# Kernel optimization log

Hardware: AMD Instinct MI355X
Metric: run time of the kernel (lower is better)

Reference implementation:

```python
import jax, jax.numpy as jnp
import numpy as np

B, T, I, H, O = 64, 1024, 512, 768, 512


def setup_inputs() -> dict:
    key = jax.random.key(0)
    ks = jax.random.split(key, 8)
    x_seq = jax.random.normal(ks[0], (B, T, I), dtype=jnp.float32)
    s = 0.02
    # Gate order along the 4H axis: f, i, g, o (matches the torch module's gates).
    Wx_f = jax.random.normal(ks[1], (4 * H, I), dtype=jnp.float32) * s
    Wh_f = jax.random.normal(ks[2], (4 * H, H), dtype=jnp.float32) * s
    Wx_b = jax.random.normal(ks[3], (4 * H, I), dtype=jnp.float32) * s
    Wh_b = jax.random.normal(ks[4], (4 * H, H), dtype=jnp.float32) * s
    # forget-gate bias init to 1.0 (f_Wxf.bias / b_Wxf.bias), rest 0
    b_gate = jnp.concatenate([jnp.ones((H,), jnp.float32), jnp.zeros((3 * H,), jnp.float32)])
    b_f = b_gate
    b_b = b_gate
    Why = jax.random.normal(ks[5], (O, 2 * H), dtype=jnp.float32) * s
    by = jnp.zeros((O,), jnp.float32)
    return {"x_seq": x_seq, "Wx_f": Wx_f, "Wh_f": Wh_f, "b_f": b_f,
            "Wx_b": Wx_b, "Wh_b": Wh_b, "b_b": b_b, "Why": Why, "by": by}


def _lstm_dir(x, Wx, Wh, b):
    # Precompute all input-to-gate projections in one fused GEMM over time.
    xp = jnp.einsum('bti,gi->btg', x, Wx) + b  # (B, T, 4H)

    def step(carry, xp_t):
        h, c = carry
        z = xp_t + h @ Wh.T                     # (B, 4H)
        f = jax.nn.sigmoid(z[:, 0 * H:1 * H])
        i = jax.nn.sigmoid(z[:, 1 * H:2 * H])
        g = jnp.tanh(z[:, 2 * H:3 * H])
        o = jax.nn.sigmoid(z[:, 3 * H:4 * H])
        c = f * c + i * g
        h = o * jnp.tanh(c)
        return (h, c), None

    h0 = jnp.zeros((x.shape[0], H), x.dtype)
    c0 = jnp.zeros((x.shape[0], H), x.dtype)
    (h, c), _ = jax.lax.scan(step, (h0, c0), jnp.swapaxes(xp, 0, 1))
    return h, c


def reference(x_seq, Wx_f, Wh_f, b_f, Wx_b, Wh_b, b_b, Why, by):
    h_fwd, c_fwd = _lstm_dir(x_seq, Wx_f, Wh_f, b_f)
    h_bwd, c_bwd = _lstm_dir(x_seq[:, ::-1, :], Wx_b, Wh_b, b_b)
    h_combined = jnp.concatenate([h_fwd, h_bwd], axis=1)  # (B, 2H)
    out = h_combined @ Why.T + by
    return out, h_fwd, c_fwd, h_bwd, c_bwd
```

## Files before the change

kernel.cpp:

```cpp
#include <hip/hip_runtime.h>
#include <hip/hip_cooperative_groups.h>

namespace cg = cooperative_groups;

#define B_ 64
#define T_ 1024
#define I_ 512
#define H_ 768
#define O_ 512
#define G4 3072
#define JB 16
#define NJ 48
#define NWGS 192

typedef short short8 __attribute__((ext_vector_type(8)));
typedef float f32x4 __attribute__((ext_vector_type(4)));
typedef int int4v __attribute__((ext_vector_type(4)));
typedef unsigned long long u64;

#define XBF_BYTES  (67108864)
#define WCAT_BYTES (15728640)
#define HBUF_BYTES (393216)

__device__ __forceinline__ unsigned short f32_to_bf16(float f) {
    union { float f; unsigned int u; } v; v.f = f;
    unsigned int r = v.u + 0x7fffu + ((v.u >> 16) & 1u);
    return (unsigned short)(r >> 16);
}
__device__ __forceinline__ float sigmoid_f(float x) { return 1.0f / (1.0f + __expf(-x)); }
__device__ __forceinline__ float tanh_f(float x) {
    float e = __expf(2.0f * x);
    return 1.0f - 2.0f / (e + 1.0f);
}

__device__ __forceinline__ void glds16(const void* g, void* l) {
    __builtin_amdgcn_global_load_lds(
        (const __attribute__((address_space(1))) unsigned int*)g,
        (__attribute__((address_space(3))) unsigned int*)l, 16, 0, 0);
}

__device__ __forceinline__ void ldsbar() {
    asm volatile("s_waitcnt lgkmcnt(0)" ::: "memory");
    __builtin_amdgcn_sched_barrier(0);
    __builtin_amdgcn_s_barrier();
    __builtin_amdgcn_sched_barrier(0);
}

__global__ void prep_x_kernel(const float* __restrict__ x, unsigned short* __restrict__ xb) {
    const size_t n = (size_t)B_ * T_ * 64;
    for (size_t i = (size_t)blockIdx.x * blockDim.x + threadIdx.x; i < n;
         i += (size_t)gridDim.x * blockDim.x) {
        int b  = (int)(i >> 16);
        int t  = (int)((i >> 6) & 1023);
        int kb = (int)(i & 63);
        const float4 v0 = *(const float4*)(x + i * 8);
        const float4 v1 = *(const float4*)(x + i * 8 + 4);
        short8 o;
        o[0] = (short)f32_to_bf16(v0.x); o[1] = (short)f32_to_bf16(v0.y);
        o[2] = (short)f32_to_bf16(v0.z); o[3] = (short)f32_to_bf16(v0.w);
        o[4] = (short)f32_to_bf16(v1.x); o[5] = (short)f32_to_bf16(v1.y);
        o[6] = (short)f32_to_bf16(v1.z); o[7] = (short)f32_to_bf16(v1.w);
        *(short8*)(xb + (((size_t)t * 64 + kb) * 64 + b) * 8) = o;
    }
}

__global__ void prep_w_kernel(const float* __restrict__ Wx_f, const float* __restrict__ Wh_f,
                              const float* __restrict__ Wx_b, const float* __restrict__ Wh_b,
                              unsigned short* __restrict__ w2, unsigned short* __restrict__ h2,
                              unsigned* __restrict__ bar) {
    const size_t n = (size_t)2 * G4 * 160;
    for (size_t i = (size_t)blockIdx.x * blockDim.x + threadIdx.x; i < n;
         i += (size_t)gridDim.x * blockDim.x) {
        int dir = (int)(i / 491520);
        int r2  = (int)(i % 491520);
        int row = r2 / 160;
        int kb  = r2 % 160;
        const float* Wx = dir ? Wx_b : Wx_f;
        const float* Wh = dir ? Wh_b : Wh_f;
        const float* src = (kb < 64) ? (Wx + (size_t)row * I_ + kb * 8)
                                     : (Wh + (size_t)row * H_ + (kb - 64) * 8);
        const float4 v0 = *(const float4*)(src);
        const float4 v1 = *(const float4*)(src + 4);
        short8 o;
        o[0] = (short)f32_to_bf16(v0.x); o[1] = (short)f32_to_bf16(v0.y);
        o[2] = (short)f32_to_bf16(v0.z); o[3] = (short)f32_to_bf16(v0.w);
        o[4] = (short)f32_to_bf16(v1.x); o[5] = (short)f32_to_bf16(v1.y);
        o[6] = (short)f32_to_bf16(v1.z); o[7] = (short)f32_to_bf16(v1.w);
        *(short8*)(w2 + (((size_t)dir * 160 + kb) * G4 + row) * 8) = o;
        if (i < 24576) {
            short8 z = {0,0,0,0,0,0,0,0};
            *(short8*)(h2 + i * 8) = z;
        }
        if (i < 512) bar[i] = 0u;
    }
}

__global__ void __launch_bounds__(512, 2)
bilstm_kernel(const float* __restrict__ bias_f, const float* __restrict__ bias_b,
              const unsigned short* __restrict__ xb, const unsigned short* __restrict__ w2,
              unsigned short* h2, unsigned* bar, float* d_out) {
    __shared__ unsigned short x_lds[64 * 32 * 8];
    __shared__ unsigned short h_lds[96 * 32 * 8];
    __shared__ float z_lds[4][32][17];
    __shared__ float c_tile[32][16];

    const int tid   = threadIdx.x;
    const int wg    = blockIdx.x;
    const int dir   = wg / 96;
    const int rem   = wg % 96;
    const int bh    = rem / NJ;
    const int jb    = rem % NJ;
    const int j0    = jb * JB;
    const int wave  = tid >> 6;
    const int lane  = tid & 63;
    const int gate  = wave & 3;
    const int mhalf = wave >> 2;
    const int quad  = lane >> 4;
    const int lrow  = lane & 15;
    const int m0l   = mhalf * 16 + lrow;

    c_tile[tid >> 4][tid & 15] = 0.0f;

    const float bias_r = (dir ? bias_b : bias_f)[gate * H_ + j0 + lrow];
    const int wrow = gate * H_ + j0 + lrow;

    const unsigned short* wx = w2 + (((size_t)dir * 160 + quad) * G4 + wrow) * 8;
    short8 wh[24];
#pragma unroll
    for (int ks = 0; ks < 24; ++ks)
        wh[ks] = *(const short8*)(w2 + (((size_t)dir * 160 + 64 + ks * 4 + quad) * G4 + wrow) * 8);

    const int group = dir * 2 + bh;
    unsigned* mybar = bar + (group * 4 + (jb & 3)) * 32;
    unsigned* barbase = bar + group * 4 * 32;

    const int src_off = (tid >> 5) * 1024 + bh * 512 + (tid & 31) * 16;

    char* const lds_wb   = (char*)x_lds + wave * 1024;
    char* const lds_mine = (char*)h_lds + tid * 16;
    const unsigned short* vax = x_lds + quad * 256 + m0l * 8;
    const unsigned short* vah = h_lds + quad * 256 + m0l * 8;

    {
        const int tx0 = dir ? (T_ - 1) : 0;
        const char* xsrc = (const char*)(xb + (size_t)tx0 * 32768) + src_off;
#pragma unroll
        for (int k = 0; k < 4; ++k) glds16(xsrc + k * 16384, lds_wb + k * 8192);
    }
    __syncthreads();

    for (int t = 0; t < T_; ++t) {
        const int pb = (t + 1) & 1;
        const int cb = t & 1;

        f32x4 acc0; acc0[0] = bias_r; acc0[1] = bias_r; acc0[2] = bias_r; acc0[3] = bias_r;

#pragma unroll
        for (int ks = 0; ks < 16; ++ks) {
            short8 a0 = *(const short8*)(vax + ks * 1024);
            short8 bf = *(const short8*)(wx + (size_t)ks * 4 * G4 * 8);
            acc0 = __builtin_amdgcn_mfma_f32_16x16x32_bf16(a0, bf, acc0, 0, 0, 0);
        }

        if (tid == 0) {
            const unsigned tgt = (unsigned)(NJ * t);
            for (;;) {
                unsigned ssum = 0;
#pragma unroll
                for (int i = 0; i < 4; ++i)
                    ssum += __hip_atomic_load(barbase + i * 32, __ATOMIC_RELAXED,
                                              __HIP_MEMORY_SCOPE_AGENT);
                if (ssum >= tgt) break;
                __builtin_amdgcn_s_sleep(1);
            }
        }
        asm volatile("" ::: "memory");
        __syncthreads();

        {
            const char* hp = (const char*)(h2 + (size_t)(dir * 2 + pb) * 49152) + src_off;
            int4v u0, u1, u2, u3, u4, u5;
#define HL(n) asm volatile("global_load_dwordx4 %0, %1, off sc1" : "=v"(u##n) : "v"(hp + (n) * 16384))
#define HS(n) *(int4v*)(lds_mine + (n) * 8192) = u##n
            HL(0); HL(1); HL(2); HL(3); HL(4); HL(5);
            asm volatile("s_waitcnt vmcnt(5)" ::: "memory"); HS(0);
            asm volatile("s_waitcnt vmcnt(4)" ::: "memory"); HS(1);
            asm volatile("s_waitcnt vmcnt(3)" ::: "memory"); HS(2);
            asm volatile("s_waitcnt vmcnt(2)" ::: "memory"); HS(3);
            asm volatile("s_waitcnt vmcnt(1)" ::: "memory"); HS(4);
            asm volatile("s_waitcnt vmcnt(0)" ::: "memory"); HS(5);
#undef HL
#undef HS
        }

        if (t + 1 < T_) {
            const int tx2 = dir ? (T_ - 2 - t) : (t + 1);
            const char* xsrc = (const char*)(xb + (size_t)tx2 * 32768) + src_off;
#pragma unroll
            for (int k = 0; k < 4; ++k) glds16(xsrc + k * 16384, lds_wb + k * 8192);
        }
        ldsbar();

#pragma unroll
        for (int ks = 0; ks < 24; ++ks) {
            short8 a0 = *(const short8*)(vah + ks * 1024);
            acc0 = __builtin_amdgcn_mfma_f32_16x16x32_bf16(a0, wh[ks], acc0, 0, 0, 0);
        }

#pragma unroll
        for (int r = 0; r < 4; ++r)
            z_lds[gate][mhalf * 16 + quad * 4 + r][lrow] = acc0[r];
        ldsbar();

        {
            unsigned short* hw = h2 + (size_t)(dir * 2 + cb) * 49152;
            const int gb  = tid >> 4;
            const int gj  = tid & 15;
            const int gjj = j0 + gj;
            const int bg  = bh * 32 + gb;
            float f0 = sigmoid_f(z_lds[0][gb][gj]);
            float i0 = sigmoid_f(z_lds[1][gb][gj]);
            float g0 = tanh_f(z_lds[2][gb][gj]);
            float o0 = sigmoid_f(z_lds[3][gb][gj]);
            float c0 = f0 * c_tile[gb][gj] + i0 * g0;
            c_tile[gb][gj] = c0;
            float h0 = o0 * tanh_f(c0);
            unsigned hv = (unsigned)f32_to_bf16(h0);
            unsigned ov = __shfl_xor(hv, 1);
            if (!(gj & 1)) {
                unsigned pack = hv | (ov << 16);
                unsigned* dst = (unsigned*)(hw + ((gjj >> 3) * 64 + bg) * 8 + (gjj & 7));
                __hip_atomic_store(dst, pack, __ATOMIC_RELAXED, __HIP_MEMORY_SCOPE_AGENT);
            }
            if (t == T_ - 1) {
                int hoff = 32768 + dir * 98304;
                d_out[hoff + bg * H_ + gjj]         = h0;
                d_out[hoff + 49152 + bg * H_ + gjj] = c0;
            }
        }
        __syncthreads();

        if (tid == 0)
            __hip_atomic_fetch_add(mybar, 1u, __ATOMIC_RELAXED, __HIP_MEMORY_SCOPE_AGENT);
    }
}

__global__ void proj_kernel(float* __restrict__ out, const float* __restrict__ Why,
                            const float* __restrict__ by) {
    __shared__ float hc[2 * H_];
    int b = blockIdx.x;
    const float* hf = out + 32768 + b * H_;
    const float* hb = out + 32768 + 98304 + b * H_;
    for (int i = threadIdx.x; i < H_; i += 256) { hc[i] = hf[i]; hc[H_ + i] = hb[i]; }
    __syncthreads();
    for (int o = threadIdx.x; o < O_; o += 256) {
        const float* wr = Why + (size_t)o * (2 * H_);
        float s = by[o];
        for (int k = 0; k < 2 * H_; k += 4) {
            float4 w = *(const float4*)(wr + k);
            s += w.x * hc[k] + w.y * hc[k + 1] + w.z * hc[k + 2] + w.w * hc[k + 3];
        }
        out[b * O_ + o] = s;
    }
}

extern "C" void kernel_launch(void* const* d_in, const int* in_sizes, int n_in,
                              void* d_out, int out_size, void* d_ws, size_t ws_size,
                              hipStream_t stream) {
    const float* x    = (const float*)d_in[0];
    const float* Wx_f = (const float*)d_in[1];
    const float* Wh_f = (const float*)d_in[2];
    const float* b_f  = (const float*)d_in[3];
    const float* Wx_b = (const float*)d_in[4];
    const float* Wh_b = (const float*)d_in[5];
    const float* b_b  = (const float*)d_in[6];
    const float* Why  = (const float*)d_in[7];
    const float* by   = (const float*)d_in[8];
    float* out = (float*)d_out;

    char* ws = (char*)d_ws;
    unsigned short* xbp = (unsigned short*)(ws);
    unsigned short* w2  = (unsigned short*)(ws + XBF_BYTES);
    unsigned short* h2  = (unsigned short*)(ws + XBF_BYTES + WCAT_BYTES);
    unsigned*       bar = (unsigned*)(ws + XBF_BYTES + WCAT_BYTES + HBUF_BYTES);

    prep_x_kernel<<<8192, 256, 0, stream>>>(x, xbp);
    prep_w_kernel<<<4096, 256, 0, stream>>>(Wx_f, Wh_f, Wx_b, Wh_b, w2, h2, bar);

    void* args[] = {(void*)&b_f, (void*)&b_b, (void*)&xbp, (void*)&w2,
                    (void*)&h2, (void*)&bar, (void*)&out};
    hipLaunchCooperativeKernel((void*)bilstm_kernel, dim3(NWGS), dim3(512), args, 0, stream);

    proj_kernel<<<B_, 256, 0, stream>>>(out, Why, by);
}
```

Baseline: 3.024 ms.

## Repartition BiLSTM workgroups into 16-batch by 32-unit tiles with split accumulators

Each workgroup now handles 16 batch rows and 32 hidden units across all four gates, instead of 32 batch rows and 16 units. That gives 8 independent groups (2 directions by 4 batch quarters), each synchronised by a 24-workgroup barrier instead of 48, and halves the recurrent h data each workgroup loads per step. The x-projection MFMAs are split around the barrier wait and the h global loads so they overlap the spin and load latency. Two accumulators alternate to break the MFMA dependency chain. In exchange, each workgroup now reads 128 weight rows spread across the four gate blocks.

```diff
diff --git a/kernel.cpp b/kernel.cpp
--- a/kernel.cpp
+++ b/kernel.cpp
@@ -9,14 +9,13 @@
 #define H_ 768
 #define O_ 512
 #define G4 3072
-#define JB 16
-#define NJ 48
+#define JB 32
+#define NJG 24
 #define NWGS 192
 
 typedef short short8 __attribute__((ext_vector_type(8)));
 typedef float f32x4 __attribute__((ext_vector_type(4)));
 typedef int int4v __attribute__((ext_vector_type(4)));
-typedef unsigned long long u64;
 
 #define XBF_BYTES  (67108864)
 #define WCAT_BYTES (15728640)
@@ -91,7 +90,7 @@
             short8 z = {0,0,0,0,0,0,0,0};
             *(short8*)(h2 + i * 8) = z;
         }
-        if (i < 512) bar[i] = 0u;
+        if (i < 1024) bar[i] = 0u;
     }
 }
 
@@ -99,30 +98,28 @@
 bilstm_kernel(const float* __restrict__ bias_f, const float* __restrict__ bias_b,
               const unsigned short* __restrict__ xb, const unsigned short* __restrict__ w2,
               unsigned short* h2, unsigned* bar, float* d_out) {
-    __shared__ unsigned short x_lds[64 * 32 * 8];
-    __shared__ unsigned short h_lds[96 * 32 * 8];
-    __shared__ float z_lds[4][32][17];
-    __shared__ float c_tile[32][16];
+    __shared__ unsigned short x_lds[64 * 16 * 8];
+    __shared__ unsigned short h_lds[96 * 16 * 8];
+    __shared__ float z_lds[16][132];
+    __shared__ float c_tile[16][32];
 
     const int tid   = threadIdx.x;
     const int wg    = blockIdx.x;
-    const int dir   = wg / 96;
-    const int rem   = wg % 96;
-    const int bh    = rem / NJ;
-    const int jb    = rem % NJ;
+    const int group = wg & 7;
+    const int jb    = wg >> 3;
+    const int dir   = group >> 2;
+    const int bq    = group & 3;
     const int j0    = jb * JB;
-    const int wave  = tid >> 6;
+    const int nt    = tid >> 6;
     const int lane  = tid & 63;
-    const int gate  = wave & 3;
-    const int mhalf = wave >> 2;
     const int quad  = lane >> 4;
     const int lrow  = lane & 15;
-    const int m0l   = mhalf * 16 + lrow;
-
-    c_tile[tid >> 4][tid & 15] = 0.0f;
-
-    const float bias_r = (dir ? bias_b : bias_f)[gate * H_ + j0 + lrow];
-    const int wrow = gate * H_ + j0 + lrow;
+    const int rl    = nt * 16 + lrow;
+
+    c_tile[tid >> 5][tid & 31] = 0.0f;
+
+    const int wrow = (rl >> 5) * H_ + j0 + (rl & 31);
+    const float bias_r = (dir ? bias_b : bias_f)[wrow];
 
     const unsigned short* wx = w2 + (((size_t)dir * 160 + quad) * G4 + wrow) * 8;
     short8 wh[24];
@@ -130,22 +127,21 @@
     for (int ks = 0; ks < 24; ++ks)
         wh[ks] = *(const short8*)(w2 + (((size_t)dir * 160 + 64 + ks * 4 + quad) * G4 + wrow) * 8);
 
-    const int group = dir * 2 + bh;
     unsigned* mybar = bar + (group * 4 + (jb & 3)) * 32;
-    unsigned* barbase = bar + group * 4 * 32;
-
-    const int src_off = (tid >> 5) * 1024 + bh * 512 + (tid & 31) * 16;
-
-    char* const lds_wb   = (char*)x_lds + wave * 1024;
-    char* const lds_mine = (char*)h_lds + tid * 16;
-    const unsigned short* vax = x_lds + quad * 256 + m0l * 8;
-    const unsigned short* vah = h_lds + quad * 256 + m0l * 8;
+    unsigned* barbase = bar + group * 128;
+
+    const int src_off = (tid >> 4) * 1024 + bq * 256 + (tid & 15) * 16;
+
+    char* const xdst = (char*)x_lds + nt * 1024;
+    char* const hdst = (char*)h_lds + tid * 16;
+    const unsigned short* vax = x_lds + quad * 128 + lrow * 8;
+    const unsigned short* vah = h_lds + quad * 128 + lrow * 8;
 
     {
         const int tx0 = dir ? (T_ - 1) : 0;
-        const char* xsrc = (const char*)(xb + (size_t)tx0 * 32768) + src_off;
-#pragma unroll
-        for (int k = 0; k < 4; ++k) glds16(xsrc + k * 16384, lds_wb + k * 8192);
+        const char* xs = (const char*)xb + (size_t)tx0 * 65536 + src_off;
+        glds16(xs, xdst);
+        glds16(xs + 32768, xdst + 8192);
     }
     __syncthreads();
 
@@ -154,16 +150,10 @@
         const int cb = t & 1;
 
         f32x4 acc0; acc0[0] = bias_r; acc0[1] = bias_r; acc0[2] = bias_r; acc0[3] = bias_r;
-
-#pragma unroll
-        for (int ks = 0; ks < 16; ++ks) {
-            short8 a0 = *(const short8*)(vax + ks * 1024);
-            short8 bf = *(const short8*)(wx + (size_t)ks * 4 * G4 * 8);
-            acc0 = __builtin_amdgcn_mfma_f32_16x16x32_bf16(a0, bf, acc0, 0, 0, 0);
-        }
-
-        if (tid == 0) {
-            const unsigned tgt = (unsigned)(NJ * t);
+        f32x4 acc1; acc1[0] = 0.f; acc1[1] = 0.f; acc1[2] = 0.f; acc1[3] = 0.f;
+
+        if (tid == 0 && t) {
+            const unsigned tgt = (unsigned)(NJG * t);
             for (;;) {
                 unsigned ssum = 0;
 #pragma unroll
@@ -174,68 +164,83 @@
                 __builtin_amdgcn_s_sleep(1);
             }
         }
+#pragma unroll
+        for (int ks = 0; ks < 8; ++ks) {
+            short8 a0 = *(const short8*)(vax + ks * 512);
+            short8 bf = *(const short8*)(wx + (size_t)ks * 4 * G4 * 8);
+            if (ks & 1) acc1 = __builtin_amdgcn_mfma_f32_16x16x32_bf16(a0, bf, acc1, 0, 0, 0);
+            else        acc0 = __builtin_amdgcn_mfma_f32_16x16x32_bf16(a0, bf, acc0, 0, 0, 0);
+        }
         asm volatile("" ::: "memory");
         __syncthreads();
 
-        {
-            const char* hp = (const char*)(h2 + (size_t)(dir * 2 + pb) * 49152) + src_off;
-            int4v u0, u1, u2, u3, u4, u5;
-#define HL(n) asm volatile("global_load_dwordx4 %0, %1, off sc1" : "=v"(u##n) : "v"(hp + (n) * 16384))
-#define HS(n) *(int4v*)(lds_mine + (n) * 8192) = u##n
-            HL(0); HL(1); HL(2); HL(3); HL(4); HL(5);
-            asm volatile("s_waitcnt vmcnt(5)" ::: "memory"); HS(0);
-            asm volatile("s_waitcnt vmcnt(4)" ::: "memory"); HS(1);
-            asm volatile("s_waitcnt vmcnt(3)" ::: "memory"); HS(2);
-            asm volatile("s_waitcnt vmcnt(2)" ::: "memory"); HS(3);
-            asm volatile("s_waitcnt vmcnt(1)" ::: "memory"); HS(4);
-            asm volatile("s_waitcnt vmcnt(0)" ::: "memory"); HS(5);
-#undef HL
-#undef HS
-        }
+        const char* hp = (const char*)h2 + (size_t)(dir * 2 + pb) * 98304 + src_off;
+        int4v u0, u1, u2;
+        asm volatile("global_load_dwordx4 %0, %1, off sc1" : "=v"(u0) : "v"(hp));
+        asm volatile("global_load_dwordx4 %0, %1, off sc1" : "=v"(u1) : "v"(hp + 32768));
+        asm volatile("global_load_dwordx4 %0, %1, off sc1" : "=v"(u2) : "v"(hp + 65536));
+
+#pragma unroll
+        for (int ks = 8; ks < 16; ++ks) {
+            short8 a0 = *(const short8*)(vax + ks * 512);
+            short8 bf = *(const short8*)(wx + (size_t)ks * 4 * G4 * 8);
+            if (ks & 1) acc1 = __builtin_amdgcn_mfma_f32_16x16x32_bf16(a0, bf, acc1, 0, 0, 0);
+            else        acc0 = __builtin_amdgcn_mfma_f32_16x16x32_bf16(a0, bf, acc0, 0, 0, 0);
+        }
+
+        asm volatile("s_waitcnt vmcnt(2)" ::: "memory");
+        *(int4v*)(hdst) = u0;
+        asm volatile("s_waitcnt vmcnt(1)" ::: "memory");
+        *(int4v*)(hdst + 8192) = u1;
+        asm volatile("s_waitcnt vmcnt(0)" ::: "memory");
+        *(int4v*)(hdst + 16384) = u2;
+
+        ldsbar();
 
         if (t + 1 < T_) {
             const int tx2 = dir ? (T_ - 2 - t) : (t + 1);
-            const char* xsrc = (const char*)(xb + (size_t)tx2 * 32768) + src_off;
-#pragma unroll
-            for (int k = 0; k < 4; ++k) glds16(xsrc + k * 16384, lds_wb + k * 8192);
-        }
-        ldsbar();
+            const char* xs = (const char*)xb + (size_t)tx2 * 65536 + src_off;
+            glds16(xs, xdst);
+            glds16(xs + 32768, xdst + 8192);
+        }
 
 #pragma unroll
         for (int ks = 0; ks < 24; ++ks) {
-            short8 a0 = *(const short8*)(vah + ks * 1024);
-            acc0 = __builtin_amdgcn_mfma_f32_16x16x32_bf16(a0, wh[ks], acc0, 0, 0, 0);
-        }
+            short8 a0 = *(const short8*)(vah + ks * 512);
+            if (ks & 1) acc1 = __builtin_amdgcn_mfma_f32_16x16x32_bf16(a0, wh[ks], acc1, 0, 0, 0);
+            else        acc0 = __builtin_amdgcn_mfma_f32_16x16x32_bf16(a0, wh[ks], acc0, 0, 0, 0);
+        }
+        f32x4 zv = acc0 + acc1;
 
 #pragma unroll
         for (int r = 0; r < 4; ++r)
-            z_lds[gate][mhalf * 16 + quad * 4 + r][lrow] = acc0[r];
+            z_lds[quad * 4 + r][rl] = zv[r];
         ldsbar();
 
         {
             unsigned short* hw = h2 + (size_t)(dir * 2 + cb) * 49152;
-            const int gb  = tid >> 4;
-            const int gj  = tid & 15;
-            const int gjj = j0 + gj;
-            const int bg  = bh * 32 + gb;
-            float f0 = sigmoid_f(z_lds[0][gb][gj]);
-            float i0 = sigmoid_f(z_lds[1][gb][gj]);
-            float g0 = tanh_f(z_lds[2][gb][gj]);
-            float o0 = sigmoid_f(z_lds[3][gb][gj]);
-            float c0 = f0 * c_tile[gb][gj] + i0 * g0;
-            c_tile[gb][gj] = c0;
+            const int b  = tid >> 5;
+            const int jl = tid & 31;
+            const int jg = j0 + jl;
+            const int bg = bq * 16 + b;
+            float f0 = sigmoid_f(z_lds[b][jl]);
+            float i0 = sigmoid_f(z_lds[b][32 + jl]);
+            float g0 = tanh_f(z_lds[b][64 + jl]);
+            float o0 = sigmoid_f(z_lds[b][96 + jl]);
+            float c0 = f0 * c_tile[b][jl] + i0 * g0;
+            c_tile[b][jl] = c0;
             float h0 = o0 * tanh_f(c0);
             unsigned hv = (unsigned)f32_to_bf16(h0);
             unsigned ov = __shfl_xor(hv, 1);
-            if (!(gj & 1)) {
+            if (!(jl & 1)) {
                 unsigned pack = hv | (ov << 16);
-                unsigned* dst = (unsigned*)(hw + ((gjj >> 3) * 64 + bg) * 8 + (gjj & 7));
+                unsigned* dst = (unsigned*)(hw + ((jg >> 3) * 64 + bg) * 8 + (jg & 7));
                 __hip_atomic_store(dst, pack, __ATOMIC_RELAXED, __HIP_MEMORY_SCOPE_AGENT);
             }
             if (t == T_ - 1) {
                 int hoff = 32768 + dir * 98304;
-                d_out[hoff + bg * H_ + gjj]         = h0;
-                d_out[hoff + 49152 + bg * H_ + gjj] = c0;
+                d_out[hoff + bg * H_ + jg]         = h0;
+                d_out[hoff + 49152 + bg * H_ + jg] = c0;
             }
         }
         __syncthreads();
```

After: 4.376 ms. 44.7% more time.

## Keep Wx in registers, split accumulators, overlap h loads with x MFMAs

Applied to the files above, without the earlier changes.

Input-projection weights (Wx) are now preloaded into registers once, so the inner loop no longer reads them from global memory every timestep. Launch bounds drop to one block per CU to make room for the extra registers. The x-projection MFMAs are split around the barrier spin and the h-state global loads, so that matrix math overlaps with the spin-wait and the load latency. Two interleaved accumulators break the MFMA dependency chain. The costs are higher register pressure, lower occupancy, and one more LDS barrier placed before the next x prefetch.

```diff
diff --git a/kernel.cpp b/kernel.cpp
--- a/kernel.cpp
+++ b/kernel.cpp
@@ -16,7 +16,6 @@
 typedef short short8 __attribute__((ext_vector_type(8)));
 typedef float f32x4 __attribute__((ext_vector_type(4)));
 typedef int int4v __attribute__((ext_vector_type(4)));
-typedef unsigned long long u64;
 
 #define XBF_BYTES  (67108864)
 #define WCAT_BYTES (15728640)
@@ -95,7 +94,7 @@
     }
 }
 
-__global__ void __launch_bounds__(512, 2)
+__global__ void __launch_bounds__(512, 1)
 bilstm_kernel(const float* __restrict__ bias_f, const float* __restrict__ bias_b,
               const unsigned short* __restrict__ xb, const unsigned short* __restrict__ w2,
               unsigned short* h2, unsigned* bar, float* d_out) {
@@ -124,7 +123,10 @@
     const float bias_r = (dir ? bias_b : bias_f)[gate * H_ + j0 + lrow];
     const int wrow = gate * H_ + j0 + lrow;
 
-    const unsigned short* wx = w2 + (((size_t)dir * 160 + quad) * G4 + wrow) * 8;
+    short8 wxr[16];
+#pragma unroll
+    for (int ks = 0; ks < 16; ++ks)
+        wxr[ks] = *(const short8*)(w2 + (((size_t)dir * 160 + ks * 4 + quad) * G4 + wrow) * 8);
     short8 wh[24];
 #pragma unroll
     for (int ks = 0; ks < 24; ++ks)
@@ -154,15 +156,9 @@
         const int cb = t & 1;
 
         f32x4 acc0; acc0[0] = bias_r; acc0[1] = bias_r; acc0[2] = bias_r; acc0[3] = bias_r;
-
-#pragma unroll
-        for (int ks = 0; ks < 16; ++ks) {
-            short8 a0 = *(const short8*)(vax + ks * 1024);
-            short8 bf = *(const short8*)(wx + (size_t)ks * 4 * G4 * 8);
-            acc0 = __builtin_amdgcn_mfma_f32_16x16x32_bf16(a0, bf, acc0, 0, 0, 0);
-        }
-
-        if (tid == 0) {
+        f32x4 acc1; acc1[0] = 0.f; acc1[1] = 0.f; acc1[2] = 0.f; acc1[3] = 0.f;
+
+        if (tid == 0 && t) {
             const unsigned tgt = (unsigned)(NJ * t);
             for (;;) {
                 unsigned ssum = 0;
@@ -174,24 +170,45 @@
                 __builtin_amdgcn_s_sleep(1);
             }
         }
+#pragma unroll
+        for (int ks = 0; ks < 8; ++ks) {
+            short8 a0 = *(const short8*)(vax + ks * 1024);
+            if (ks & 1) acc1 = __builtin_amdgcn_mfma_f32_16x16x32_bf16(a0, wxr[ks], acc1, 0, 0, 0);
+            else        acc0 = __builtin_amdgcn_mfma_f32_16x16x32_bf16(a0, wxr[ks], acc0, 0, 0, 0);
+        }
         asm volatile("" ::: "memory");
         __syncthreads();
 
-        {
-            const char* hp = (const char*)(h2 + (size_t)(dir * 2 + pb) * 49152) + src_off;
-            int4v u0, u1, u2, u3, u4, u5;
-#define HL(n) asm volatile("global_load_dwordx4 %0, %1, off sc1" : "=v"(u##n) : "v"(hp + (n) * 16384))
-#define HS(n) *(int4v*)(lds_mine + (n) * 8192) = u##n
-            HL(0); HL(1); HL(2); HL(3); HL(4); HL(5);
-            asm volatile("s_waitcnt vmcnt(5)" ::: "memory"); HS(0);
-            asm volatile("s_waitcnt vmcnt(4)" ::: "memory"); HS(1);
-            asm volatile("s_waitcnt vmcnt(3)" ::: "memory"); HS(2);
-            asm volatile("s_waitcnt vmcnt(2)" ::: "memory"); HS(3);
-            asm volatile("s_waitcnt vmcnt(1)" ::: "memory"); HS(4);
-            asm volatile("s_waitcnt vmcnt(0)" ::: "memory"); HS(5);
-#undef HL
-#undef HS
-        }
+        const char* hp = (const char*)(h2 + (size_t)(dir * 2 + pb) * 49152) + src_off;
+        int4v u0, u1, u2, u3, u4, u5;
+        asm volatile("global_load_dwordx4 %0, %1, off sc1" : "=v"(u0) : "v"(hp));
+        asm volatile("global_load_dwordx4 %0, %1, off sc1" : "=v"(u1) : "v"(hp + 16384));
+        asm volatile("global_load_dwordx4 %0, %1, off sc1" : "=v"(u2) : "v"(hp + 32768));
+        asm volatile("global_load_dwordx4 %0, %1, off sc1" : "=v"(u3) : "v"(hp + 49152));
+        asm volatile("global_load_dwordx4 %0, %1, off sc1" : "=v"(u4) : "v"(hp + 65536));
+        asm volatile("global_load_dwordx4 %0, %1, off sc1" : "=v"(u5) : "v"(hp + 81920));
+
+#pragma unroll
+        for (int ks = 8; ks < 16; ++ks) {
+            short8 a0 = *(const short8*)(vax + ks * 1024);
+            if (ks & 1) acc1 = __builtin_amdgcn_mfma_f32_16x16x32_bf16(a0, wxr[ks], acc1, 0, 0, 0);
+            else        acc0 = __builtin_amdgcn_mfma_f32_16x16x32_bf16(a0, wxr[ks], acc0, 0, 0, 0);
+        }
+
+        asm volatile("s_waitcnt vmcnt(5)" ::: "memory");
+        *(int4v*)(lds_mine) = u0;
+        asm volatile("s_waitcnt vmcnt(4)" ::: "memory");
+        *(int4v*)(lds_mine + 8192) = u1;
+        asm volatile("s_waitcnt vmcnt(3)" ::: "memory");
+        *(int4v*)(lds_mine + 16384) = u2;
+        asm volatile("s_waitcnt vmcnt(2)" ::: "memory");
+        *(int4v*)(lds_mine + 24576) = u3;
+        asm volatile("s_waitcnt vmcnt(1)" ::: "memory");
+        *(int4v*)(lds_mine + 32768) = u4;
+        asm volatile("s_waitcnt vmcnt(0)" ::: "memory");
+        *(int4v*)(lds_mine + 40960) = u5;
+
+        ldsbar();
 
         if (t + 1 < T_) {
             const int tx2 = dir ? (T_ - 2 - t) : (t + 1);
@@ -199,17 +216,18 @@
 #pragma unroll
             for (int k = 0; k < 4; ++k) glds16(xsrc + k * 16384, lds_wb + k * 8192);
         }
-        ldsbar();
 
 #pragma unroll
         for (int ks = 0; ks < 24; ++ks) {
             short8 a0 = *(const short8*)(vah + ks * 1024);
-            acc0 = __builtin_amdgcn_mfma_f32_16x16x32_bf16(a0, wh[ks], acc0, 0, 0, 0);
-        }
+            if (ks & 1) acc1 = __builtin_amdgcn_mfma_f32_16x16x32_bf16(a0, wh[ks], acc1, 0, 0, 0);
+            else        acc0 = __builtin_amdgcn_mfma_f32_16x16x32_bf16(a0, wh[ks], acc0, 0, 0, 0);
+        }
+        f32x4 zv = acc0 + acc1;
 
 #pragma unroll
         for (int r = 0; r < 4; ++r)
-            z_lds[gate][mhalf * 16 + quad * 4 + r][lrow] = acc0[r];
+            z_lds[gate][mhalf * 16 + quad * 4 + r][lrow] = zv[r];
         ldsbar();
 
         {
```

Result: slower. 3.334 ms (+10.2%).

## Split K across waves with all four gates per wave, reduce partials in LDS

Applied to the files above, without the earlier changes.

Each wave now owns a quarter of the K dimension and computes all four gate tiles, instead of one gate over the full K. The A fragment is reused across four MFMAs, so each wave issues a quarter as many LDS reads. Partial sums go to a larger LDS buffer and are summed before the activations. The recurrent weights are no longer held in registers; they are reloaded from global or L2 every timestep, which adds memory traffic on the serial critical path.

```diff
diff --git a/kernel.cpp b/kernel.cpp
--- a/kernel.cpp
+++ b/kernel.cpp
@@ -16,7 +16,6 @@
 typedef short short8 __attribute__((ext_vector_type(8)));
 typedef float f32x4 __attribute__((ext_vector_type(4)));
 typedef int int4v __attribute__((ext_vector_type(4)));
-typedef unsigned long long u64;
 
 #define XBF_BYTES  (67108864)
 #define WCAT_BYTES (15728640)
@@ -101,7 +100,7 @@
               unsigned short* h2, unsigned* bar, float* d_out) {
     __shared__ unsigned short x_lds[64 * 32 * 8];
     __shared__ unsigned short h_lds[96 * 32 * 8];
-    __shared__ float z_lds[4][32][17];
+    __shared__ float z_part[4][4][32][20];
     __shared__ float c_tile[32][16];
 
     const int tid   = threadIdx.x;
@@ -113,7 +112,7 @@
     const int j0    = jb * JB;
     const int wave  = tid >> 6;
     const int lane  = tid & 63;
-    const int gate  = wave & 3;
+    const int kq    = wave & 3;
     const int mhalf = wave >> 2;
     const int quad  = lane >> 4;
     const int lrow  = lane & 15;
@@ -121,14 +120,17 @@
 
     c_tile[tid >> 4][tid & 15] = 0.0f;
 
-    const float bias_r = (dir ? bias_b : bias_f)[gate * H_ + j0 + lrow];
-    const int wrow = gate * H_ + j0 + lrow;
-
-    const unsigned short* wx = w2 + (((size_t)dir * 160 + quad) * G4 + wrow) * 8;
-    short8 wh[24];
-#pragma unroll
-    for (int ks = 0; ks < 24; ++ks)
-        wh[ks] = *(const short8*)(w2 + (((size_t)dir * 160 + 64 + ks * 4 + quad) * G4 + wrow) * 8);
+    const float* bias = dir ? bias_b : bias_f;
+    const float biasF = kq ? 0.0f : bias[0 * H_ + j0 + lrow];
+    const float biasI = kq ? 0.0f : bias[1 * H_ + j0 + lrow];
+    const float biasG = kq ? 0.0f : bias[2 * H_ + j0 + lrow];
+    const float biasO = kq ? 0.0f : bias[3 * H_ + j0 + lrow];
+
+    const size_t WKB = (size_t)G4 * 8;
+    const unsigned short* wxb = w2 + ((size_t)(dir * 160) + kq * 16 + quad) * WKB
+                                   + (size_t)(j0 + lrow) * 8;
+    const unsigned short* whb = w2 + ((size_t)(dir * 160 + 64) + kq * 24 + quad) * WKB
+                                   + (size_t)(j0 + lrow) * 8;
 
     const int group = dir * 2 + bh;
     unsigned* mybar = bar + (group * 4 + (jb & 3)) * 32;
@@ -138,8 +140,8 @@
 
     char* const lds_wb   = (char*)x_lds + wave * 1024;
     char* const lds_mine = (char*)h_lds + tid * 16;
-    const unsigned short* vax = x_lds + quad * 256 + m0l * 8;
-    const unsigned short* vah = h_lds + quad * 256 + m0l * 8;
+    const unsigned short* vax = x_lds + ((kq * 16 + quad) * 32 + m0l) * 8;
+    const unsigned short* vah = h_lds + ((kq * 24 + quad) * 32 + m0l) * 8;
 
     {
         const int tx0 = dir ? (T_ - 1) : 0;
@@ -153,13 +155,22 @@
         const int pb = (t + 1) & 1;
         const int cb = t & 1;
 
-        f32x4 acc0; acc0[0] = bias_r; acc0[1] = bias_r; acc0[2] = bias_r; acc0[3] = bias_r;
-
-#pragma unroll
-        for (int ks = 0; ks < 16; ++ks) {
+        f32x4 accF; accF[0] = biasF; accF[1] = biasF; accF[2] = biasF; accF[3] = biasF;
+        f32x4 accI; accI[0] = biasI; accI[1] = biasI; accI[2] = biasI; accI[3] = biasI;
+        f32x4 accG; accG[0] = biasG; accG[1] = biasG; accG[2] = biasG; accG[3] = biasG;
+        f32x4 accO; accO[0] = biasO; accO[1] = biasO; accO[2] = biasO; accO[3] = biasO;
+
+#pragma unroll
+        for (int ks = 0; ks < 4; ++ks) {
             short8 a0 = *(const short8*)(vax + ks * 1024);
-            short8 bf = *(const short8*)(wx + (size_t)ks * 4 * G4 * 8);
-            acc0 = __builtin_amdgcn_mfma_f32_16x16x32_bf16(a0, bf, acc0, 0, 0, 0);
+            short8 b0 = *(const short8*)(wxb + (size_t)ks * 4 * WKB);
+            short8 b1 = *(const short8*)(wxb + (size_t)ks * 4 * WKB + 1 * H_ * 8);
+            short8 b2 = *(const short8*)(wxb + (size_t)ks * 4 * WKB + 2 * H_ * 8);
+            short8 b3 = *(const short8*)(wxb + (size_t)ks * 4 * WKB + 3 * H_ * 8);
+            accF = __builtin_amdgcn_mfma_f32_16x16x32_bf16(a0, b0, accF, 0, 0, 0);
+            accI = __builtin_amdgcn_mfma_f32_16x16x32_bf16(a0, b1, accI, 0, 0, 0);
+            accG = __builtin_amdgcn_mfma_f32_16x16x32_bf16(a0, b2, accG, 0, 0, 0);
+            accO = __builtin_amdgcn_mfma_f32_16x16x32_bf16(a0, b3, accO, 0, 0, 0);
         }
 
         if (tid == 0) {
@@ -202,14 +213,28 @@
         ldsbar();
 
 #pragma unroll
-        for (int ks = 0; ks < 24; ++ks) {
+        for (int ks = 0; ks < 6; ++ks) {
             short8 a0 = *(const short8*)(vah + ks * 1024);
-            acc0 = __builtin_amdgcn_mfma_f32_16x16x32_bf16(a0, wh[ks], acc0, 0, 0, 0);
-        }
-
-#pragma unroll
-        for (int r = 0; r < 4; ++r)
-            z_lds[gate][mhalf * 16 + quad * 4 + r][lrow] = acc0[r];
+            short8 b0 = *(const short8*)(whb + (size_t)ks * 4 * WKB);
+            short8 b1 = *(const short8*)(whb + (size_t)ks * 4 * WKB + 1 * H_ * 8);
+            short8 b2 = *(const short8*)(whb + (size_t)ks * 4 * WKB + 2 * H_ * 8);
+            short8 b3 = *(const short8*)(whb + (size_t)ks * 4 * WKB + 3 * H_ * 8);
+            accF = __builtin_amdgcn_mfma_f32_16x16x32_bf16(a0, b0, accF, 0, 0, 0);
+            accI = __builtin_amdgcn_mfma_f32_16x16x32_bf16(a0, b1, accI, 0, 0, 0);
+            accG = __builtin_amdgcn_mfma_f32_16x16x32_bf16(a0, b2, accG, 0, 0, 0);
+            accO = __builtin_amdgcn_mfma_f32_16x16x32_bf16(a0, b3, accO, 0, 0, 0);
+        }
+
+        {
+            const int zr = mhalf * 16 + quad * 4;
+#pragma unroll
+            for (int r = 0; r < 4; ++r) {
+                z_part[kq][0][zr + r][lrow] = accF[r];
+                z_part[kq][1][zr + r][lrow] = accI[r];
+                z_part[kq][2][zr + r][lrow] = accG[r];
+                z_part[kq][3][zr + r][lrow] = accO[r];
+            }
+        }
         ldsbar();
 
         {
@@ -218,10 +243,18 @@
             const int gj  = tid & 15;
             const int gjj = j0 + gj;
             const int bg  = bh * 32 + gb;
-            float f0 = sigmoid_f(z_lds[0][gb][gj]);
-            float i0 = sigmoid_f(z_lds[1][gb][gj]);
-            float g0 = tanh_f(z_lds[2][gb][gj]);
-            float o0 = sigmoid_f(z_lds[3][gb][gj]);
+            float zf = z_part[0][0][gb][gj] + z_part[1][0][gb][gj]
+                     + z_part[2][0][gb][gj] + z_part[3][0][gb][gj];
+            float zi = z_part[0][1][gb][gj] + z_part[1][1][gb][gj]
+                     + z_part[2][1][gb][gj] + z_part[3][1][gb][gj];
+            float zg = z_part[0][2][gb][gj] + z_part[1][2][gb][gj]
+                     + z_part[2][2][gb][gj] + z_part[3][2][gb][gj];
+            float zo = z_part[0][3][gb][gj] + z_part[1][3][gb][gj]
+                     + z_part[2][3][gb][gj] + z_part[3][3][gb][gj];
+            float f0 = sigmoid_f(zf);
+            float i0 = sigmoid_f(zi);
+            float g0 = tanh_f(zg);
+            float o0 = sigmoid_f(zo);
             float c0 = f0 * c_tile[gb][gj] + i0 * g0;
             c_tile[gb][gj] = c0;
             float h0 = o0 * tanh_f(c0);
```

Result: slower. 4.323 ms (+42.9%).
